# Performance work log

Hardware: AMD Instinct MI355X
Metric: run time of the kernel (lower is better)

Reference implementation:

```python
import jax, jax.numpy as jnp
import numpy as np

TOKENS, D_MODEL, N_EXPERTS, K = 16384, 4096, 64, 2


def setup_inputs() -> dict:
    key = jax.random.key(0)
    kx, kw, kb = jax.random.split(key, 3)
    x = jax.random.normal(kx, (TOKENS, D_MODEL), dtype=jnp.float32)
    # nn.Linear(input_dim, num_experts): weight [num_experts, input_dim], bias [num_experts]
    bound = 1.0 / np.sqrt(D_MODEL)
    W = jax.random.uniform(kw, (N_EXPERTS, D_MODEL), minval=-bound, maxval=bound, dtype=jnp.float32)
    b = jax.random.uniform(kb, (N_EXPERTS,), minval=-bound, maxval=bound, dtype=jnp.float32)
    return {"x": x, "W": W, "b": b}


def reference(x, W, b):
    # logits = x @ W.T + b ; softmax over experts ; top-k
    logits = jnp.einsum('td,ed->te', x, W) + b  # [tokens, experts]
    scores = jax.nn.softmax(logits, axis=-1)
    topk_scores, topk_indices = jax.lax.top_k(scores, K)
    return (topk_indices, topk_scores)
```

## Files before the change

### kernel.cpp

```cpp
#include <hip/hip_runtime.h>
#include <hip/hip_bf16.h>
#include <cstdint>
#include <cstddef>

#define TOKENS 16384
#define DMODEL 4096
#define NEXP   64
#define NWIN   16
#define WINK   256
#define NKC2   128

typedef __attribute__((ext_vector_type(8))) short bf16x8;
typedef __attribute__((ext_vector_type(4))) float f32x4;

__device__ __forceinline__ void cvt_hilo8(const float f[8], bf16x8* hi, bf16x8* lo) {
  union { __hip_bfloat16 b; unsigned short u; } cv;
  bf16x8 hv, lv;
#pragma unroll
  for (int j = 0; j < 8; ++j) {
    __hip_bfloat16 hb = __float2bfloat16(f[j]);
    cv.b = hb; hv[j] = (short)cv.u;
    float r = f[j] - __bfloat162float(hb);
    cv.b = __float2bfloat16(r); lv[j] = (short)cv.u;
  }
  *hi = hv; *lo = lv;
}

__global__ __launch_bounds__(256)
void prep_W(const float* __restrict__ W, uint4* __restrict__ wh, uint4* __restrict__ wl) {
  const int tid = blockIdx.x * 256 + threadIdx.x;
  const int l   = tid & 63;
  const int eg  = (tid >> 6) & 3;
  const int kc2 = tid >> 8;
  const int e   = eg * 16 + (l & 15);
  const int k   = kc2 * 32 + (l >> 4) * 8;
  const float* src = W + (size_t)e * DMODEL + k;
  float f[8];
#pragma unroll
  for (int j = 0; j < 8; ++j) f[j] = src[j];
  bf16x8 hi, lo;
  cvt_hilo8(f, &hi, &lo);
  const int slot = (kc2 * 4 + eg) * 64 + l;
  wh[slot] = __builtin_bit_cast(uint4, hi);
  wl[slot] = __builtin_bit_cast(uint4, lo);
}

__device__ __forceinline__ int xaddr(int s) {
  return (s * 16) ^ (((s >> 7) & 7) << 4);
}

__device__ __forceinline__ void loadx4(const float* __restrict__ x, int t0, int w, int l,
                                       int win, float4 L[8]) {
#pragma unroll
  for (int j = 0; j < 4; ++j) {
    const float* p = x + (size_t)(t0 + w * 8 + 2 * j + (l >> 5)) * DMODEL
                       + win * WINK + (l & 31) * 8;
    L[j * 2]     = *(const float4*)p;
    L[j * 2 + 1] = *(const float4*)(p + 4);
  }
}

__device__ __forceinline__ void cvtwrite(char* hb, char* lb, int w, int l,
                                         const float4 L[8]) {
  const int kc2l = (l & 31) >> 2;
  const int ksub = l & 3;
  const int mt   = w >> 1;
#pragma unroll
  for (int j = 0; j < 4; ++j) {
    const int r  = w * 8 + 2 * j + (l >> 5);
    const int lp = (r & 15) + ksub * 16;
    const int a  = xaddr((kc2l * 2 + mt) * 64 + lp);
    float f[8] = {L[j*2].x, L[j*2].y, L[j*2].z, L[j*2].w,
                  L[j*2+1].x, L[j*2+1].y, L[j*2+1].z, L[j*2+1].w};
    bf16x8 hi, lo;
    cvt_hilo8(f, &hi, &lo);
    *(bf16x8*)(hb + a) = hi;
    *(bf16x8*)(lb + a) = lo;
  }
}

__device__ __forceinline__ void compute_win(const char* hb, const char* lb, int wi, int l,
    const uint4* __restrict__ whp, const uint4* __restrict__ wlp,
    uint4 (&ph)[2], uint4 (&pl)[2], f32x4& acc0, f32x4& acc1) {
#pragma unroll
  for (int c = 0; c < 8; ++c) {
    uint4 bhu = ph[c & 1], blu = pl[c & 1];
    const int kci = wi * 8 + c;
    if (kci + 2 < NKC2) {
      ph[c & 1] = whp[(kci + 2) * 256];
      pl[c & 1] = wlp[(kci + 2) * 256];
    }
    const int s0 = (c * 2 + 0) * 64 + l;
    const int s1 = (c * 2 + 1) * 64 + l;
    bf16x8 ah0 = *(const bf16x8*)(hb + xaddr(s0));
    bf16x8 ah1 = *(const bf16x8*)(hb + xaddr(s1));
    bf16x8 al0 = *(const bf16x8*)(lb + xaddr(s0));
    bf16x8 al1 = *(const bf16x8*)(lb + xaddr(s1));
    bf16x8 bh = __builtin_bit_cast(bf16x8, bhu);
    bf16x8 bl = __builtin_bit_cast(bf16x8, blu);
    acc0 = __builtin_amdgcn_mfma_f32_16x16x32_bf16(ah0, bh, acc0, 0, 0, 0);
    acc1 = __builtin_amdgcn_mfma_f32_16x16x32_bf16(ah1, bh, acc1, 0, 0, 0);
    acc0 = __builtin_amdgcn_mfma_f32_16x16x32_bf16(ah0, bl, acc0, 0, 0, 0);
    acc1 = __builtin_amdgcn_mfma_f32_16x16x32_bf16(ah1, bl, acc1, 0, 0, 0);
    acc0 = __builtin_amdgcn_mfma_f32_16x16x32_bf16(al0, bh, acc0, 0, 0, 0);
    acc1 = __builtin_amdgcn_mfma_f32_16x16x32_bf16(al1, bh, acc1, 0, 0, 0);
  }
}

__global__ __launch_bounds__(256, 2)
void gemm_topk(const float* __restrict__ x, const uint4* __restrict__ whB,
               const uint4* __restrict__ wlB, const float* __restrict__ b,
               float* __restrict__ out) {
  __shared__ __align__(16) char lds[65536];
  const int tid = threadIdx.x;
  const int l   = tid & 63;
  const int w   = tid >> 6;
  const int t0  = blockIdx.x * 32;

  char* h0 = lds;              char* l0 = lds + 16384;
  char* h1 = lds + 32768;      char* l1 = lds + 49152;
  const uint4* whp = whB + w * 64 + l;
  const uint4* wlp = wlB + w * 64 + l;

  f32x4 acc0 = {0.f, 0.f, 0.f, 0.f}, acc1 = {0.f, 0.f, 0.f, 0.f};
  float4 LR0[8], LR1[8];

  loadx4(x, t0, w, l, 0, LR0);
  cvtwrite(h0, l0, w, l, LR0);
  loadx4(x, t0, w, l, 1, LR1);
  uint4 ph[2], pl[2];
  ph[0] = whp[0];   pl[0] = wlp[0];
  ph[1] = whp[256]; pl[1] = wlp[256];
  __syncthreads();

  for (int wi = 0; wi < NWIN; wi += 2) {
    if (wi + 2 < NWIN) loadx4(x, t0, w, l, wi + 2, LR0);
    cvtwrite(h1, l1, w, l, LR1);
    compute_win(h0, l0, wi, l, whp, wlp, ph, pl, acc0, acc1);
    __syncthreads();
    if (wi + 3 < NWIN) loadx4(x, t0, w, l, wi + 3, LR1);
    if (wi + 2 < NWIN) cvtwrite(h0, l0, w, l, LR0);
    compute_win(h1, l1, wi + 1, l, whp, wlp, ph, pl, acc0, acc1);
    __syncthreads();
  }

  float* red = (float*)lds;
  const float bias = b[w * 16 + (l & 15)];
#pragma unroll
  for (int reg = 0; reg < 4; ++reg) {
    const int tr = (l >> 4) * 4 + reg;
    red[tr * 66 + w * 16 + (l & 15)]        = acc0[reg] + bias;
    red[(16 + tr) * 66 + w * 16 + (l & 15)] = acc1[reg] + bias;
  }
  __syncthreads();

#pragma unroll
  for (int i = 0; i < 8; ++i) {
    const int tl = w * 8 + i;
    const float v = red[tl * 66 + l];

    float m1 = v; int i1 = l;
#pragma unroll
    for (int off = 32; off > 0; off >>= 1) {
      float ov = __shfl_xor(m1, off, 64);
      int   oi = __shfl_xor(i1, off, 64);
      if (ov > m1 || (ov == m1 && oi < i1)) { m1 = ov; i1 = oi; }
    }
    float v2 = (l == i1) ? -__builtin_inff() : v;
    float m2 = v2; int i2 = l;
#pragma unroll
    for (int off = 32; off > 0; off >>= 1) {
      float ov = __shfl_xor(m2, off, 64);
      int   oi = __shfl_xor(i2, off, 64);
      if (ov > m2 || (ov == m2 && oi < i2)) { m2 = ov; i2 = oi; }
    }
    float e = __expf(v - m1);
#pragma unroll
    for (int off = 32; off > 0; off >>= 1) e += __shfl_xor(e, off, 64);

    if (l == 0) {
      const int t = t0 + tl;
      out[(size_t)t * 2 + 0] = (float)i1;
      out[(size_t)t * 2 + 1] = (float)i2;
      float inv = 1.0f / e;
      out[(size_t)TOKENS * 2 + (size_t)t * 2 + 0] = inv;
      out[(size_t)TOKENS * 2 + (size_t)t * 2 + 1] = __expf(m2 - m1) * inv;
    }
  }
}

extern "C" void kernel_launch(void* const* d_in, const int* in_sizes, int n_in,
                              void* d_out, int out_size, void* d_ws, size_t ws_size,
                              hipStream_t stream) {
  const float* x = (const float*)d_in[0];
  const float* W = (const float*)d_in[1];
  const float* b = (const float*)d_in[2];
  float* out = (float*)d_out;

  uint4* wh = (uint4*)d_ws;
  uint4* wl = wh + 32768;

  hipLaunchKernelGGL(prep_W,    dim3(128),         dim3(256), 0, stream, W, wh, wl);
  hipLaunchKernelGGL(gemm_topk, dim3(TOKENS / 32), dim3(256), 0, stream, x, wh, wl, b, out);
}
```

Measured before the change: 85.94 us.

## Stage x into LDS with async global-to-LDS loads and convert at use

Tokens are now copied straight from global memory into a swizzled fp32 LDS buffer with global_load_lds, instead of loading into registers, splitting into bf16 hi/lo and writing both halves to LDS. The hi/lo split moves into the MFMA loop, where each wave converts the A fragments it reads. The aim is to drop the register staging and VALU work from the load path so more x traffic stays in flight and overlaps with compute. In exchange, each of the four waves repeats the conversion of the same x tile, and LDS reads double in width because they are now fp32.

```diff
diff --git a/kernel.cpp b/kernel.cpp
--- a/kernel.cpp
+++ b/kernel.cpp
@@ -6,12 +6,18 @@
 #define TOKENS 16384
 #define DMODEL 4096
 #define NEXP   64
-#define NWIN   16
 #define WINK   256
-#define NKC2   128
+#define NWIN   (DMODEL / WINK)
+#define NKC2   (DMODEL / 32)
 
 typedef __attribute__((ext_vector_type(8))) short bf16x8;
 typedef __attribute__((ext_vector_type(4))) float f32x4;
+
+__device__ __forceinline__ void gld_lds16(const float* g, void* l) {
+  __builtin_amdgcn_global_load_lds(
+      (__attribute__((address_space(1))) const void*)g,
+      (__attribute__((address_space(3))) void*)l, 16, 0, 0);
+}
 
 __device__ __forceinline__ void cvt_hilo8(const float f[8], bf16x8* hi, bf16x8* lo) {
   union { __hip_bfloat16 b; unsigned short u; } cv;
@@ -45,68 +51,6 @@
   wl[slot] = __builtin_bit_cast(uint4, lo);
 }
 
-__device__ __forceinline__ int xaddr(int s) {
-  return (s * 16) ^ (((s >> 7) & 7) << 4);
-}
-
-__device__ __forceinline__ void loadx4(const float* __restrict__ x, int t0, int w, int l,
-                                       int win, float4 L[8]) {
-#pragma unroll
-  for (int j = 0; j < 4; ++j) {
-    const float* p = x + (size_t)(t0 + w * 8 + 2 * j + (l >> 5)) * DMODEL
-                       + win * WINK + (l & 31) * 8;
-    L[j * 2]     = *(const float4*)p;
-    L[j * 2 + 1] = *(const float4*)(p + 4);
-  }
-}
-
-__device__ __forceinline__ void cvtwrite(char* hb, char* lb, int w, int l,
-                                         const float4 L[8]) {
-  const int kc2l = (l & 31) >> 2;
-  const int ksub = l & 3;
-  const int mt   = w >> 1;
-#pragma unroll
-  for (int j = 0; j < 4; ++j) {
-    const int r  = w * 8 + 2 * j + (l >> 5);
-    const int lp = (r & 15) + ksub * 16;
-    const int a  = xaddr((kc2l * 2 + mt) * 64 + lp);
-    float f[8] = {L[j*2].x, L[j*2].y, L[j*2].z, L[j*2].w,
-                  L[j*2+1].x, L[j*2+1].y, L[j*2+1].z, L[j*2+1].w};
-    bf16x8 hi, lo;
-    cvt_hilo8(f, &hi, &lo);
-    *(bf16x8*)(hb + a) = hi;
-    *(bf16x8*)(lb + a) = lo;
-  }
-}
-
-__device__ __forceinline__ void compute_win(const char* hb, const char* lb, int wi, int l,
-    const uint4* __restrict__ whp, const uint4* __restrict__ wlp,
-    uint4 (&ph)[2], uint4 (&pl)[2], f32x4& acc0, f32x4& acc1) {
-#pragma unroll
-  for (int c = 0; c < 8; ++c) {
-    uint4 bhu = ph[c & 1], blu = pl[c & 1];
-    const int kci = wi * 8 + c;
-    if (kci + 2 < NKC2) {
-      ph[c & 1] = whp[(kci + 2) * 256];
-      pl[c & 1] = wlp[(kci + 2) * 256];
-    }
-    const int s0 = (c * 2 + 0) * 64 + l;
-    const int s1 = (c * 2 + 1) * 64 + l;
-    bf16x8 ah0 = *(const bf16x8*)(hb + xaddr(s0));
-    bf16x8 ah1 = *(const bf16x8*)(hb + xaddr(s1));
-    bf16x8 al0 = *(const bf16x8*)(lb + xaddr(s0));
-    bf16x8 al1 = *(const bf16x8*)(lb + xaddr(s1));
-    bf16x8 bh = __builtin_bit_cast(bf16x8, bhu);
-    bf16x8 bl = __builtin_bit_cast(bf16x8, blu);
-    acc0 = __builtin_amdgcn_mfma_f32_16x16x32_bf16(ah0, bh, acc0, 0, 0, 0);
-    acc1 = __builtin_amdgcn_mfma_f32_16x16x32_bf16(ah1, bh, acc1, 0, 0, 0);
-    acc0 = __builtin_amdgcn_mfma_f32_16x16x32_bf16(ah0, bl, acc0, 0, 0, 0);
-    acc1 = __builtin_amdgcn_mfma_f32_16x16x32_bf16(ah1, bl, acc1, 0, 0, 0);
-    acc0 = __builtin_amdgcn_mfma_f32_16x16x32_bf16(al0, bh, acc0, 0, 0, 0);
-    acc1 = __builtin_amdgcn_mfma_f32_16x16x32_bf16(al1, bh, acc1, 0, 0, 0);
-  }
-}
-
 __global__ __launch_bounds__(256, 2)
 void gemm_topk(const float* __restrict__ x, const uint4* __restrict__ whB,
                const uint4* __restrict__ wlB, const float* __restrict__ b,
@@ -117,31 +61,69 @@
   const int w   = tid >> 6;
   const int t0  = blockIdx.x * 32;
 
-  char* h0 = lds;              char* l0 = lds + 16384;
-  char* h1 = lds + 32768;      char* l1 = lds + 49152;
+  char* xb0 = lds;
+  char* xb1 = lds + 32768;
   const uint4* whp = whB + w * 64 + l;
   const uint4* wlp = wlB + w * 64 + l;
 
+  auto stage = [&](int win, char* buf) {
+#pragma unroll
+    for (int p = 0; p < 8; ++p) {
+      const int r  = p * 4 + w;
+      const int sb = (l * 16) ^ ((r & 7) << 4);
+      const float* src = x + (size_t)(t0 + r) * DMODEL + win * WINK + (sb >> 2);
+      gld_lds16(src, buf + p * 4096 + tid * 16);
+    }
+  };
+
   f32x4 acc0 = {0.f, 0.f, 0.f, 0.f}, acc1 = {0.f, 0.f, 0.f, 0.f};
-  float4 LR0[8], LR1[8];
+  uint4 ph[2], pl[2];
 
-  loadx4(x, t0, w, l, 0, LR0);
-  cvtwrite(h0, l0, w, l, LR0);
-  loadx4(x, t0, w, l, 1, LR1);
-  uint4 ph[2], pl[2];
+  auto compute = [&](const char* buf, int wi) {
+#pragma unroll
+    for (int c = 0; c < 8; ++c) {
+      uint4 bhu = ph[c & 1], blu = pl[c & 1];
+      const int kci = wi * 8 + c;
+      if (kci + 2 < NKC2) {
+        ph[c & 1] = whp[(size_t)(kci + 2) * 256];
+        pl[c & 1] = wlp[(size_t)(kci + 2) * 256];
+      }
+      const int r0 = l & 15, r1 = 16 + (l & 15);
+      const int ku = c * 8 + (l >> 4) * 2;
+      const int s0 = r0 & 7;
+      float4 f00 = *(const float4*)(buf + r0 * 1024 + ((ku ^ s0) << 4));
+      float4 f01 = *(const float4*)(buf + r0 * 1024 + (((ku + 1) ^ s0) << 4));
+      float4 f10 = *(const float4*)(buf + r1 * 1024 + ((ku ^ s0) << 4));
+      float4 f11 = *(const float4*)(buf + r1 * 1024 + (((ku + 1) ^ s0) << 4));
+      float t0f[8] = {f00.x, f00.y, f00.z, f00.w, f01.x, f01.y, f01.z, f01.w};
+      float t1f[8] = {f10.x, f10.y, f10.z, f10.w, f11.x, f11.y, f11.z, f11.w};
+      bf16x8 ah0, al0, ah1, al1;
+      cvt_hilo8(t0f, &ah0, &al0);
+      cvt_hilo8(t1f, &ah1, &al1);
+      bf16x8 bh = __builtin_bit_cast(bf16x8, bhu);
+      bf16x8 bl = __builtin_bit_cast(bf16x8, blu);
+      acc0 = __builtin_amdgcn_mfma_f32_16x16x32_bf16(ah0, bh, acc0, 0, 0, 0);
+      acc1 = __builtin_amdgcn_mfma_f32_16x16x32_bf16(ah1, bh, acc1, 0, 0, 0);
+      acc0 = __builtin_amdgcn_mfma_f32_16x16x32_bf16(ah0, bl, acc0, 0, 0, 0);
+      acc1 = __builtin_amdgcn_mfma_f32_16x16x32_bf16(ah1, bl, acc1, 0, 0, 0);
+      acc0 = __builtin_amdgcn_mfma_f32_16x16x32_bf16(al0, bh, acc0, 0, 0, 0);
+      acc1 = __builtin_amdgcn_mfma_f32_16x16x32_bf16(al1, bh, acc1, 0, 0, 0);
+    }
+  };
+
+  stage(0, xb0);
   ph[0] = whp[0];   pl[0] = wlp[0];
   ph[1] = whp[256]; pl[1] = wlp[256];
   __syncthreads();
+  stage(1, xb1);
 
   for (int wi = 0; wi < NWIN; wi += 2) {
-    if (wi + 2 < NWIN) loadx4(x, t0, w, l, wi + 2, LR0);
-    cvtwrite(h1, l1, w, l, LR1);
-    compute_win(h0, l0, wi, l, whp, wlp, ph, pl, acc0, acc1);
+    compute(xb0, wi);
     __syncthreads();
-    if (wi + 3 < NWIN) loadx4(x, t0, w, l, wi + 3, LR1);
-    if (wi + 2 < NWIN) cvtwrite(h0, l0, w, l, LR0);
-    compute_win(h1, l1, wi + 1, l, whp, wlp, ph, pl, acc0, acc1);
+    if (wi + 2 < NWIN) stage(wi + 2, xb0);
+    compute(xb1, wi + 1);
     __syncthreads();
+    if (wi + 3 < NWIN) stage(wi + 3, xb1);
   }
 
   float* red = (float*)lds;
```

Result: slower. 89.01 us (+3.6%).
